# Kernel tuning notes

Measured on AMD Instinct MI355X. Metric: run time of the kernel, lower is better.

Reference implementation:

```python
import jax, jax.numpy as jnp
import numpy as np

OUT, IN = 4096, 4096      # weight_shape
VDIM = 8                  # codebook vector_dim
CODEBOOK_SIZE = 256
LEVEL = 2                 # haar_decomposition_level
INV_SQRT2 = 0.7071067811865476


def unpack_bool(packed, shape):
    # packed: int array of bytes (values 0..255); unpack 8 bits per byte (LSB first)
    bits = (packed[:, None] >> jnp.arange(8, dtype=packed.dtype)) & 1  # [n_bytes, 8]
    return bits.reshape(shape)


def inverse_haar(c, level):
    # c: [..., n] orthonormal Haar coefficients laid out [a_L, d_L, d_{L-1}, ..., d_1]
    n = c.shape[-1]
    m = n >> level
    a = c[..., :m]
    while m < n:
        d = c[..., m:2 * m]
        even = (a + d) * INV_SQRT2
        odd = (a - d) * INV_SQRT2
        a = jnp.stack([even, odd], axis=-1).reshape(c.shape[:-1] + (2 * m,))
        m *= 2
    return a


def setup_inputs() -> dict:
    key = jax.random.key(0)
    k1, k2, k3, k4, k5 = jax.random.split(key, 5)
    x = jax.random.normal(k1, (4, 2048, IN), dtype=jnp.float32)
    codebook = jax.random.normal(k2, (CODEBOOK_SIZE, VDIM), dtype=jnp.float32)
    scales = jax.random.uniform(k5, (OUT, 1), dtype=jnp.float32)
    indices = jax.random.randint(k3, (OUT * IN // VDIM,), 0, CODEBOOK_SIZE, dtype=jnp.int32)
    signs_packed = jax.random.randint(k4, (OUT * IN // 8,), 0, 256, dtype=jnp.int32)
    return {"x": x, "codebook": codebook, "scales": scales,
            "indices": indices, "signs_packed": signs_packed}


def reference(x, codebook, scales, indices, signs_packed):
    # codebook gather -> haar-domain magnitudes, reshaped to signs_shape = weight shape
    haar_freq = codebook[indices].reshape(OUT, IN)
    # unpack sign bits and map {0,1} -> {-1,+1}
    signs = 2.0 * unpack_bool(signs_packed, (OUT, IN)).astype(haar_freq.dtype) - 1.0
    haar_freq = haar_freq * signs
    # multi-level inverse Haar wavelet along in_features
    w = inverse_haar(haar_freq, LEVEL)
    w = w * scales  # per-output-row scales
    return jnp.einsum('bsi,oi->bso', x, w)
```

## Files before the change

kernel.cpp:

```cpp
#include <hip/hip_runtime.h>
#include <hip/hip_bf16.h>

typedef unsigned short u16;
typedef unsigned int u32;
typedef float f32x4 __attribute__((ext_vector_type(4)));
typedef u16 u16x4 __attribute__((ext_vector_type(4)));
typedef u16 u16x8 __attribute__((ext_vector_type(8)));
typedef __bf16 bf16x8 __attribute__((ext_vector_type(8)));

#define OUT_DIM 4096
#define IN_DIM  4096
#define M_DIM   8192

__device__ __forceinline__ u16 f2bf(float f) {
  u32 u = __builtin_bit_cast(u32, f);
  return (u16)((u + 0x7FFFu + ((u >> 16) & 1u)) >> 16);
}

__global__ __launch_bounds__(256) void build_w_kernel(
    const float* __restrict__ codebook, const float* __restrict__ scales,
    const int* __restrict__ indices, const int* __restrict__ signs,
    u16* __restrict__ W) {
  __shared__ float c[IN_DIM];
  const int o   = blockIdx.x;
  const int tid = threadIdx.x;
  for (int g = tid; g < IN_DIM / 8; g += 256) {
    const int idx = indices[o * (IN_DIM / 8) + g];
    const int sp  = signs[o * (IN_DIM / 8) + g];
    f32x4 c0 = *(const f32x4*)&codebook[idx * 8];
    f32x4 c1 = *(const f32x4*)&codebook[idx * 8 + 4];
    float v[8] = {c0[0], c0[1], c0[2], c0[3], c1[0], c1[1], c1[2], c1[3]};
#pragma unroll
    for (int j = 0; j < 8; ++j)
      c[g * 8 + j] = ((sp >> j) & 1) ? v[j] : -v[j];
  }
  __syncthreads();
  const float scale = scales[o];
  const float S = 0.70710678118654752440f;
  for (int t = tid; t < IN_DIM / 4; t += 256) {
    float a   = c[t];
    float d1  = c[IN_DIM / 4 + t];
    float d2a = c[IN_DIM / 2 + 2 * t];
    float d2b = c[IN_DIM / 2 + 2 * t + 1];
    float e  = (a + d1) * S;
    float od = (a - d1) * S;
    u16x4 w;
    w[0] = f2bf((e  + d2a) * S * scale);
    w[1] = f2bf((e  - d2a) * S * scale);
    w[2] = f2bf((od + d2b) * S * scale);
    w[3] = f2bf((od - d2b) * S * scale);
    *(u16x4*)&W[(size_t)o * IN_DIM + 4 * t] = w;
  }
}

__global__ __launch_bounds__(256) void cvt_x_kernel(
    const float* __restrict__ X, u16* __restrict__ Xb) {
  const int stride = gridDim.x * blockDim.x;
  const int n8 = (M_DIM * IN_DIM) / 8;
  for (int i = blockIdx.x * blockDim.x + threadIdx.x; i < n8; i += stride) {
    f32x4 a = *(const f32x4*)&X[(size_t)i * 8];
    f32x4 b = *(const f32x4*)&X[(size_t)i * 8 + 4];
    u16x8 r;
    r[0] = f2bf(a[0]); r[1] = f2bf(a[1]); r[2] = f2bf(a[2]); r[3] = f2bf(a[3]);
    r[4] = f2bf(b[0]); r[5] = f2bf(b[1]); r[6] = f2bf(b[2]); r[7] = f2bf(b[3]);
    *(u16x8*)&Xb[(size_t)i * 8] = r;
  }
}

__global__ __launch_bounds__(512, 2) void gemm_bt_kernel(
    const u16* __restrict__ A,
    const u16* __restrict__ B,
    float*     __restrict__ C) {
  constexpr int K    = IN_DIM;
  constexpr int NT   = K / 32;
  constexpr int BUFB = 32768;
  extern __shared__ char smem[];

  const int tid  = threadIdx.x;
  const int wave = tid >> 6;
  const int lane = tid & 63;

  const int swz = (blockIdx.x & 7) * 64 + (blockIdx.x >> 3);
  const int bm = (swz >> 4) * 256;
  const int bn = (swz & 15) * 256;

  const int wr  = (wave >> 2) * 128;
  const int wc  = (wave & 3) * 64;
  const int fr  = lane & 15;
  const int fkB = (lane >> 4) * 16;

  int offA[8], offB[4];
#pragma unroll
  for (int h = 0; h < 8; ++h) {
    int o = (wr + h * 16 + fr) * 64 + fkB;
    offA[h] = o ^ ((o >> 3) & 0x30);
  }
#pragma unroll
  for (int n = 0; n < 4; ++n) {
    int o = (wc + n * 16 + fr) * 64 + fkB;
    offB[n] = 16384 + (o ^ ((o >> 3) & 0x30));
  }

  const u16* srcA[2]; const u16* srcB[2];
#pragma unroll
  for (int i = 0; i < 2; ++i) {
    int d = i * 8192 + tid * 16;
    int l = d ^ ((d >> 3) & 0x30);
    int row = d >> 6;
    srcA[i] = A + (size_t)(bm + row) * K + ((l & 63) >> 1);
    srcB[i] = B + (size_t)(bn + row) * K + ((l & 63) >> 1);
  }
  const int ldsW = wave * 1024;

  auto stageA = [&](int tt) {
    char* base = smem + (tt & 3) * BUFB + ldsW;
#pragma unroll
    for (int i = 0; i < 2; ++i)
      __builtin_amdgcn_global_load_lds(
          (const __attribute__((address_space(1))) void*)(srcA[i] + tt * 32),
          (__attribute__((address_space(3))) void*)(base + i * 8192), 16, 0, 0);
  };
  auto stageB = [&](int tt) {
    char* base = smem + (tt & 3) * BUFB + 16384 + ldsW;
#pragma unroll
    for (int i = 0; i < 2; ++i)
      __builtin_amdgcn_global_load_lds(
          (const __attribute__((address_space(1))) void*)(srcB[i] + tt * 32),
          (__attribute__((address_space(3))) void*)(base + i * 8192), 16, 0, 0);
  };

  f32x4 acc[8][4] = {};
  bf16x8 aloX[4], bX[4], aloY[4], bY[4], ahi[4];

  stageA(0); stageB(0); stageA(1); stageB(1); stageA(2); stageB(2);
  asm volatile("s_waitcnt vmcnt(8)" ::: "memory");
  __builtin_amdgcn_s_barrier();
  {
    const char* buf0 = smem;
#pragma unroll
    for (int n = 0; n < 4; ++n) bX[n]   = *(const bf16x8*)(buf0 + offB[n]);
#pragma unroll
    for (int m = 0; m < 4; ++m) aloX[m] = *(const bf16x8*)(buf0 + offA[m]);
  }

  auto tile = [&](int t, bf16x8 (&cA)[4], bf16x8 (&cB)[4],
                  bf16x8 (&nA)[4], bf16x8 (&nB)[4]) {
    const char* buf  = smem + (t & 3) * BUFB;
    const char* bufn = smem + ((t + 1) & 3) * BUFB;
    if (t + 3 < NT) stageA(t + 3);
#pragma unroll
    for (int m = 0; m < 4; ++m) ahi[m] = *(const bf16x8*)(buf + offA[4 + m]);
    __builtin_amdgcn_s_setprio(1);
#pragma unroll
    for (int m = 0; m < 4; ++m)
#pragma unroll
      for (int n = 0; n < 4; ++n)
        acc[m][n] = __builtin_amdgcn_mfma_f32_16x16x32_bf16(cA[m], cB[n], acc[m][n], 0, 0, 0);
    __builtin_amdgcn_s_setprio(0);
    if (t + 3 < NT)       asm volatile("s_waitcnt vmcnt(6)" ::: "memory");
    else if (t + 3 == NT) asm volatile("s_waitcnt vmcnt(4)" ::: "memory");
    else if (t + 2 == NT) asm volatile("s_waitcnt vmcnt(0)" ::: "memory");
    __builtin_amdgcn_s_barrier();
    if (t + 3 < NT) stageB(t + 3);
    if (t + 1 < NT) {
#pragma unroll
      for (int n = 0; n < 4; ++n) nB[n] = *(const bf16x8*)(bufn + offB[n]);
#pragma unroll
      for (int m = 0; m < 4; ++m) nA[m] = *(const bf16x8*)(bufn + offA[m]);
    }
    __builtin_amdgcn_s_setprio(1);
#pragma unroll
    for (int m = 0; m < 4; ++m)
#pragma unroll
      for (int n = 0; n < 4; ++n)
        acc[4 + m][n] = __builtin_amdgcn_mfma_f32_16x16x32_bf16(ahi[m], cB[n], acc[4 + m][n], 0, 0, 0);
    __builtin_amdgcn_s_setprio(0);
    __builtin_amdgcn_s_barrier();
  };

  for (int t = 0; t < NT; t += 2) {
    tile(t,     aloX, bX, aloY, bY);
    tile(t + 1, aloY, bY, aloX, bX);
  }

#pragma unroll
  for (int h = 0; h < 8; ++h)
#pragma unroll
    for (int n = 0; n < 4; ++n) {
      const int col = bn + wc + n * 16 + fr;
#pragma unroll
      for (int j = 0; j < 4; ++j) {
        const int row = bm + wr + h * 16 + (lane >> 4) * 4 + j;
        C[(size_t)row * OUT_DIM + col] = acc[h][n][j];
      }
    }
}

extern "C" void kernel_launch(void* const* d_in, const int* in_sizes, int n_in,
                              void* d_out, int out_size, void* d_ws, size_t ws_size,
                              hipStream_t stream) {
  const float* x        = (const float*)d_in[0];
  const float* codebook = (const float*)d_in[1];
  const float* scales   = (const float*)d_in[2];
  const int*   indices  = (const int*)d_in[3];
  const int*   signs    = (const int*)d_in[4];
  float* out = (float*)d_out;

  u16* W  = (u16*)d_ws;
  u16* Xb = (u16*)d_ws + (size_t)OUT_DIM * IN_DIM;

  (void)hipFuncSetAttribute((const void*)gemm_bt_kernel,
                            hipFuncAttributeMaxDynamicSharedMemorySize, 131072);

  build_w_kernel<<<OUT_DIM, 256, 0, stream>>>(codebook, scales, indices, signs, W);
  cvt_x_kernel<<<2048, 256, 0, stream>>>(x, Xb);
  gemm_bt_kernel<<<(M_DIM / 256) * (OUT_DIM / 256), 512, 131072, stream>>>(Xb, W, out);
}
```

Baseline: 295.7 us.

## Collapse split-half GEMM pipeline into single-phase stage, prefetch and compute step

```diff
diff --git a/kernel.cpp b/kernel.cpp
--- a/kernel.cpp
+++ b/kernel.cpp
@@ -112,75 +112,60 @@
   }
   const int ldsW = wave * 1024;
 
-  auto stageA = [&](int tt) {
+  auto stage = [&](int tt) {
     char* base = smem + (tt & 3) * BUFB + ldsW;
 #pragma unroll
-    for (int i = 0; i < 2; ++i)
+    for (int i = 0; i < 2; ++i) {
       __builtin_amdgcn_global_load_lds(
           (const __attribute__((address_space(1))) void*)(srcA[i] + tt * 32),
           (__attribute__((address_space(3))) void*)(base + i * 8192), 16, 0, 0);
-  };
-  auto stageB = [&](int tt) {
-    char* base = smem + (tt & 3) * BUFB + 16384 + ldsW;
-#pragma unroll
-    for (int i = 0; i < 2; ++i)
       __builtin_amdgcn_global_load_lds(
           (const __attribute__((address_space(1))) void*)(srcB[i] + tt * 32),
-          (__attribute__((address_space(3))) void*)(base + i * 8192), 16, 0, 0);
+          (__attribute__((address_space(3))) void*)(base + 16384 + i * 8192), 16, 0, 0);
+    }
   };
 
   f32x4 acc[8][4] = {};
-  bf16x8 aloX[4], bX[4], aloY[4], bY[4], ahi[4];
-
-  stageA(0); stageB(0); stageA(1); stageB(1); stageA(2); stageB(2);
+  bf16x8 aX[8], bX[4], aY[8], bY[4];
+
+  stage(0); stage(1); stage(2);
   asm volatile("s_waitcnt vmcnt(8)" ::: "memory");
   __builtin_amdgcn_s_barrier();
   {
     const char* buf0 = smem;
 #pragma unroll
-    for (int n = 0; n < 4; ++n) bX[n]   = *(const bf16x8*)(buf0 + offB[n]);
-#pragma unroll
-    for (int m = 0; m < 4; ++m) aloX[m] = *(const bf16x8*)(buf0 + offA[m]);
-  }
-
-  auto tile = [&](int t, bf16x8 (&cA)[4], bf16x8 (&cB)[4],
-                  bf16x8 (&nA)[4], bf16x8 (&nB)[4]) {
-    const char* buf  = smem + (t & 3) * BUFB;
-    const char* bufn = smem + ((t + 1) & 3) * BUFB;
-    if (t + 3 < NT) stageA(t + 3);
-#pragma unroll
-    for (int m = 0; m < 4; ++m) ahi[m] = *(const bf16x8*)(buf + offA[4 + m]);
+    for (int n = 0; n < 4; ++n) bX[n] = *(const bf16x8*)(buf0 + offB[n]);
+#pragma unroll
+    for (int m = 0; m < 8; ++m) aX[m] = *(const bf16x8*)(buf0 + offA[m]);
+  }
+
+  auto tileStep = [&](int t, bf16x8 (&cA)[8], bf16x8 (&cB)[4],
+                      bf16x8 (&nA)[8], bf16x8 (&nB)[4]) {
+    if (t + 3 < NT) stage(t + 3);
+    if (t + 3 < NT)       asm volatile("s_waitcnt vmcnt(8)" ::: "memory");
+    else if (t + 3 == NT) asm volatile("s_waitcnt vmcnt(4)" ::: "memory");
+    else if (t + 2 == NT) asm volatile("s_waitcnt vmcnt(0)" ::: "memory");
+    __builtin_amdgcn_s_barrier();
+    if (t + 1 < NT) {
+      const char* bufn = smem + ((t + 1) & 3) * BUFB;
+#pragma unroll
+      for (int n = 0; n < 4; ++n) nB[n] = *(const bf16x8*)(bufn + offB[n]);
+#pragma unroll
+      for (int m = 0; m < 8; ++m) nA[m] = *(const bf16x8*)(bufn + offA[m]);
+    }
     __builtin_amdgcn_s_setprio(1);
 #pragma unroll
-    for (int m = 0; m < 4; ++m)
+    for (int m = 0; m < 8; ++m)
 #pragma unroll
       for (int n = 0; n < 4; ++n)
         acc[m][n] = __builtin_amdgcn_mfma_f32_16x16x32_bf16(cA[m], cB[n], acc[m][n], 0, 0, 0);
     __builtin_amdgcn_s_setprio(0);
-    if (t + 3 < NT)       asm volatile("s_waitcnt vmcnt(6)" ::: "memory");
-    else if (t + 3 == NT) asm volatile("s_waitcnt vmcnt(4)" ::: "memory");
-    else if (t + 2 == NT) asm volatile("s_waitcnt vmcnt(0)" ::: "memory");
-    __builtin_amdgcn_s_barrier();
-    if (t + 3 < NT) stageB(t + 3);
-    if (t + 1 < NT) {
-#pragma unroll
-      for (int n = 0; n < 4; ++n) nB[n] = *(const bf16x8*)(bufn + offB[n]);
-#pragma unroll
-      for (int m = 0; m < 4; ++m) nA[m] = *(const bf16x8*)(bufn + offA[m]);
-    }
-    __builtin_amdgcn_s_setprio(1);
-#pragma unroll
-    for (int m = 0; m < 4; ++m)
-#pragma unroll
-      for (int n = 0; n < 4; ++n)
-        acc[4 + m][n] = __builtin_amdgcn_mfma_f32_16x16x32_bf16(ahi[m], cB[n], acc[4 + m][n], 0, 0, 0);
-    __builtin_amdgcn_s_setprio(0);
     __builtin_amdgcn_s_barrier();
   };
 
   for (int t = 0; t < NT; t += 2) {
-    tile(t,     aloX, bX, aloY, bY);
-    tile(t + 1, aloY, bY, aloX, bX);
+    tileStep(t,     aX, bX, aY, bY);
+    tileStep(t + 1, aY, bY, aX, bX);
   }
 
 #pragma unroll
```

New measurement: 305.8 us. +3.4%, slower.
